# Kernel tuning notes

Hardware: AMD Instinct MI355X
Metric: run time of the kernel (lower is better)

The kernel has to match this reference:

```python
import jax, jax.numpy as jnp
import numpy as np

N_NODES = 100000
N_EDGES = 1600000
N_REL = 4
DIM = 64
N_LAYERS = 3
EPS = 1e-10


def setup_inputs() -> dict:
    key = jax.random.key(0)
    ks = jax.random.split(key, 12)
    node_feat = jax.random.normal(ks[0], (N_NODES, DIM), dtype=jnp.float32)
    edge_weight = jnp.ones((N_EDGES,), dtype=jnp.float32)
    edge_src = jax.random.randint(ks[1], (N_EDGES,), 0, N_NODES, dtype=jnp.int32)
    edge_dst = jax.random.randint(ks[2], (N_EDGES,), 0, N_NODES, dtype=jnp.int32)
    edge_rel = jax.random.randint(ks[3], (N_EDGES,), 0, N_REL, dtype=jnp.int32)
    s = 0.1
    # stacked per-layer parameters (all layers are DIM -> DIM)
    conv_lin_w = jax.random.normal(ks[4], (N_LAYERS, N_REL * DIM, DIM), dtype=jnp.float32) * s
    conv_lin_b = jnp.zeros((N_LAYERS, DIM), dtype=jnp.float32)
    conv_self_w = jax.random.normal(ks[5], (N_LAYERS, DIM, DIM), dtype=jnp.float32) * s
    conv_self_b = jnp.zeros((N_LAYERS, DIM), dtype=jnp.float32)
    hw_proj_w = jax.random.normal(ks[6], (N_LAYERS, 2 * DIM, DIM), dtype=jnp.float32) * s
    hw_proj_b = jnp.zeros((N_LAYERS, DIM), dtype=jnp.float32)
    hw_trans_w = jax.random.normal(ks[7], (N_LAYERS, 2 * DIM, DIM), dtype=jnp.float32) * s
    hw_trans_b = jnp.full((N_LAYERS, DIM), -2.0, dtype=jnp.float32)  # bias.fill_(-2.0)
    return dict(node_feat=node_feat, edge_weight=edge_weight,
                conv_lin_w=conv_lin_w, conv_lin_b=conv_lin_b,
                conv_self_w=conv_self_w, conv_self_b=conv_self_b,
                hw_proj_w=hw_proj_w, hw_proj_b=hw_proj_b,
                hw_trans_w=hw_trans_w, hw_trans_b=hw_trans_b,
                edge_src=edge_src, edge_dst=edge_dst, edge_rel=edge_rel)


def _rgcn(x, ew, src, dst, rel, lin_w, lin_b, self_w, self_b):
    # message: gather source features, weight by edge weight
    msg = x[src] * ew[:, None]                     # [E, D]
    seg = dst * N_REL + rel                        # [E] -> (node, relation) bucket
    num_seg = N_NODES * N_REL
    agg = jax.ops.segment_sum(msg, seg, num_segments=num_seg)        # [N*R, D]
    deg = jax.ops.segment_sum(ew, seg, num_segments=num_seg)         # [N*R]
    upd = (agg / (deg[:, None] + EPS)).reshape(N_NODES, N_REL * DIM)  # [N, R*D]
    out = upd @ lin_w + lin_b + x @ self_w + self_b
    return jax.nn.sigmoid(out)


def _highway(cur, prev, pw, pb, tw, tb):
    cat = jnp.concatenate([cur, prev], axis=1)     # [N, 2D]
    proj = jax.nn.relu(cat @ pw + pb)
    gate = jax.nn.sigmoid(cat @ tw + tb)
    return gate * proj + (1.0 - gate) * cur


def reference(node_feat, edge_weight, conv_lin_w, conv_lin_b, conv_self_w, conv_self_b,
              hw_proj_w, hw_proj_b, hw_trans_w, hw_trans_b, edge_src, edge_dst, edge_rel):
    layer_input = node_feat
    prev_gcn = node_feat
    for i in range(N_LAYERS):
        hidden = _rgcn(layer_input, edge_weight, edge_src, edge_dst, edge_rel,
                       conv_lin_w[i], conv_lin_b[i], conv_self_w[i], conv_self_b[i])
        gated = _highway(hidden, prev_gcn, hw_proj_w[i], hw_proj_b[i],
                         hw_trans_w[i], hw_trans_b[i])
        layer_input = gated
        prev_gcn = hidden
    return layer_input  # node_feature
```

## Files before the change

kernel.cpp:

```cpp
#include <hip/hip_runtime.h>

#define NN   100000
#define NE   1600000
#define NB   400000
#define EPS  1e-10f

#define NPB   32
#define NCHK  256
#define EPC   6250
#define NBUCK 391
#define NHBC  (NBUCK * NCHK)
#define NSCAN (NB + NHBC)
#define NBLK_FUSED 489
#define KB_CAP 4608

typedef __attribute__((ext_vector_type(8))) short bfrag8;
typedef __attribute__((ext_vector_type(4))) float f4acc;

__device__ __forceinline__ unsigned short f2bf(float f) {
    union { float f; unsigned u; } v; v.f = f;
    unsigned r = v.u + 0x7FFF + ((v.u >> 16) & 1);
    return (unsigned short)(r >> 16);
}
__device__ __forceinline__ float bf2f(unsigned short b) {
    union { unsigned u; float f; } v; v.u = ((unsigned)b) << 16;
    return v.f;
}

__global__ __launch_bounds__(256) void kA1(
    const int* __restrict__ dst, const int* __restrict__ rel,
    int* __restrict__ cnt_seg, int* __restrict__ histBC,
    const float* __restrict__ xf, unsigned short* __restrict__ xb)
{
    __shared__ int s_h[NBUCK];
    for (int i = threadIdx.x; i < NBUCK; i += 256) s_h[i] = 0;
    __syncthreads();
    int e0 = blockIdx.x * EPC;
    for (int e = e0 + threadIdx.x; e < e0 + EPC; e += 256) {
        int d = dst[e];
        atomicAdd(&s_h[d >> 8], 1);
        atomicAdd(&cnt_seg[d * 4 + rel[e]], 1);
    }
    __syncthreads();
    for (int i = threadIdx.x; i < NBUCK; i += 256)
        histBC[i * NCHK + blockIdx.x] = s_h[i];

    for (int c = blockIdx.x * 256 + threadIdx.x; c < NN * 8; c += NCHK * 256) {
        const float4* s4 = (const float4*)xf + (size_t)c * 2;
        float4 a = s4[0], b = s4[1];
        unsigned short r[8] = { f2bf(a.x), f2bf(a.y), f2bf(a.z), f2bf(a.w),
                                f2bf(b.x), f2bf(b.y), f2bf(b.z), f2bf(b.w) };
        *(uint4*)(xb + (size_t)c * 8) = *(const uint4*)r;
    }
}

__global__ __launch_bounds__(1024) void k_scan_local_g(
    const int* __restrict__ in, int* __restrict__ out,
    int* __restrict__ blksum, int n)
{
    __shared__ int s[1024];
    int t = threadIdx.x;
    int i = blockIdx.x * 1024 + t;
    int v = (i < n) ? in[i] : 0;
    s[t] = v;
    __syncthreads();
    #pragma unroll
    for (int off = 1; off < 1024; off <<= 1) {
        int u = (t >= off) ? s[t - off] : 0;
        __syncthreads();
        s[t] += u;
        __syncthreads();
    }
    if (i < n) out[i] = s[t] - v;
    if (t == 1023) blksum[blockIdx.x] = s[t];
}

__global__ __launch_bounds__(512) void k_scan_blk_g(
    int* __restrict__ blksum, int* __restrict__ blkoff, int nblk)
{
    __shared__ int s[512];
    int t = threadIdx.x;
    int v = (t < nblk) ? blksum[t] : 0;
    s[t] = v;
    __syncthreads();
    #pragma unroll
    for (int off = 1; off < 512; off <<= 1) {
        int u = (t >= off) ? s[t - off] : 0;
        __syncthreads();
        s[t] += u;
        __syncthreads();
    }
    if (t < nblk) blkoff[t] = s[t] - v;
}

__global__ __launch_bounds__(1024) void k_scan_add_g(
    int* __restrict__ out, const int* __restrict__ blkoff, int n)
{
    int i = blockIdx.x * 1024 + threadIdx.x;
    if (i < n) out[i] += blkoff[blockIdx.x];
}

__global__ __launch_bounds__(256) void kA3(
    const int* __restrict__ src, const int* __restrict__ dst,
    const int* __restrict__ rel, const float* __restrict__ ew,
    const int* __restrict__ chunkOff, int2* __restrict__ pA)
{
    __shared__ int s_c[NBUCK];
    for (int i = threadIdx.x; i < NBUCK; i += 256)
        s_c[i] = chunkOff[i * NCHK + blockIdx.x] - NE;
    __syncthreads();
    int e0 = blockIdx.x * EPC;
    for (int e = e0 + threadIdx.x; e < e0 + EPC; e += 256) {
        int d = dst[e], r = rel[e];
        int pos = atomicAdd(&s_c[d >> 8], 1);
        int2 v;
        v.x = src[e] | (((d & 255) * 4 + r) << 20);
        v.y = __float_as_int(ew[e]);
        pA[pos] = v;
    }
}

__global__ __launch_bounds__(256) void kB(
    const int* __restrict__ row_ptr, const int2* __restrict__ pA,
    int2* __restrict__ edat)
{
    __shared__ int2 s_e[KB_CAP];
    __shared__ int s_c[1024];
    __shared__ int s_p[256];
    const int b    = blockIdx.x;
    const int t    = threadIdx.x;
    const int seg0 = b * 1024;
    const int segN = min(1024, NB - seg0);
    const int pbeg = row_ptr[seg0];
    const int pend = row_ptr[seg0 + segN];

    for (int i = t; i < 1024; i += 256) s_c[i] = 0;
    __syncthreads();
    for (int p = pbeg + t; p < pend; p += 256) {
        int2 v = pA[p];
        int idx = p - pbeg;
        if (idx < KB_CAP) s_e[idx] = v;
        atomicAdd(&s_c[((unsigned)v.x) >> 20], 1);
    }
    __syncthreads();

    int c0 = s_c[t * 4], c1 = s_c[t * 4 + 1], c2 = s_c[t * 4 + 2], c3 = s_c[t * 4 + 3];
    int tsum = c0 + c1 + c2 + c3;
    s_p[t] = tsum;
    __syncthreads();
    #pragma unroll
    for (int off = 1; off < 256; off <<= 1) {
        int u = (t >= off) ? s_p[t - off] : 0;
        __syncthreads();
        s_p[t] += u;
        __syncthreads();
    }
    int base = s_p[t] - tsum;
    s_c[t * 4]     = base;
    s_c[t * 4 + 1] = base + c0;
    s_c[t * 4 + 2] = base + c0 + c1;
    s_c[t * 4 + 3] = base + c0 + c1 + c2;
    __syncthreads();

    for (int p = pbeg + t; p < pend; p += 256) {
        int idx = p - pbeg;
        int2 v = (idx < KB_CAP) ? s_e[idx] : pA[p];
        int sl = ((unsigned)v.x) >> 20;
        int pos = atomicAdd(&s_c[sl], 1);
        int2 o; o.x = v.x & 0xFFFFF; o.y = v.y;
        edat[pbeg + pos] = o;
    }
    if (b == 0 && t < 192) { int2 z; z.x = 0; z.y = 0; edat[NE + t] = z; }
}

__global__ __launch_bounds__(256) void k_cvt_w(
    const float* __restrict__ lin_w, const float* __restrict__ self_w,
    const float* __restrict__ pw, const float* __restrict__ tw,
    unsigned short* __restrict__ WL, unsigned short* __restrict__ WP,
    unsigned short* __restrict__ WT2)
{
    int id = blockIdx.x * 256 + threadIdx.x;
    if (id >= 3 * 64 * 576) return;
    int i = id / (64 * 576);
    int r = id % (64 * 576);
    int j = r / 576;
    int k = r % 576;
    if (k < 320) {
        float v = (k < 256) ? lin_w[((size_t)i * 256 + k) * 64 + j]
                            : self_w[((size_t)i * 64 + (k - 256)) * 64 + j];
        WL[((size_t)i * 64 + j) * 320 + k] = f2bf(v);
    } else if (k < 448) {
        int kk = k - 320;
        WP[((size_t)i * 64 + j) * 128 + kk] = f2bf(pw[((size_t)i * 128 + kk) * 64 + j]);
    } else {
        int kk = k - 448;
        WT2[((size_t)i * 64 + j) * 128 + kk] = f2bf(tw[((size_t)i * 128 + kk) * 64 + j]);
    }
}

template<int LBASE>
__device__ __forceinline__ void gather16(
    unsigned short (&g)[16], int2 mb,
    const unsigned short* __restrict__ xb, int lane)
{
    #pragma unroll
    for (int j = 0; j < 16; ++j) {
        unsigned sm = (unsigned)__builtin_amdgcn_readlane(mb.x, LBASE + j);
        g[j] = xb[((size_t)sm << 6) + lane];
    }
}

template<int LBASE, bool CHECK>
__device__ __forceinline__ void consume16(
    const unsigned short (&g)[16], int2 mb, int ebase,
    int E1, int& seg, int& segEnd,
    float& acc, float& dsum,
    const int* sRP, int sbase, int wid, int lane, char* sAp)
{
    #pragma unroll
    for (int j = 0; j < 16; ++j) {
        int eidx = ebase + j;
        if (!CHECK || eidx < E1) {
            while (eidx >= segEnd) {
                float u = acc * __builtin_amdgcn_rcpf(dsum + EPS);
                int ln = wid * 8 + (seg >> 2);
                int cb = ((seg & 3) * 64 + lane) * 2;
                *(unsigned short*)(sAp + ln * 640 + (cb ^ ((ln & 7) << 4))) = f2bf(u);
                acc = 0.f; dsum = 0.f;
                ++seg;
                segEnd = __builtin_amdgcn_readfirstlane(sRP[sbase + seg + 1]);
            }
            float w = __int_as_float(__builtin_amdgcn_readlane(mb.y, LBASE + j));
            acc = fmaf(bf2f(g[j]), w, acc);
            dsum += w;
        }
    }
}

template<bool CHECK>
__device__ __forceinline__ void agg_iter64(
    unsigned short (&ga)[16], unsigned short (&gb)[16],
    int2& mb, int e, int E1, int& seg, int& segEnd,
    float& acc, float& dsum, const int* sRP, int sbase,
    int wid, int lane, char* sAp,
    const unsigned short* __restrict__ xb, const int2* __restrict__ edat)
{
    int2 mbn = edat[e + 64 + lane];
    gather16<16>(gb, mb, xb, lane);
    consume16<0, CHECK>(ga, mb, e, E1, seg, segEnd, acc, dsum, sRP, sbase, wid, lane, sAp);
    gather16<32>(ga, mb, xb, lane);
    consume16<16, CHECK>(gb, mb, e + 16, E1, seg, segEnd, acc, dsum, sRP, sbase, wid, lane, sAp);
    gather16<48>(gb, mb, xb, lane);
    consume16<32, CHECK>(ga, mb, e + 32, E1, seg, segEnd, acc, dsum, sRP, sbase, wid, lane, sAp);
    gather16<0>(ga, mbn, xb, lane);
    consume16<48, CHECK>(gb, mb, e + 48, E1, seg, segEnd, acc, dsum, sRP, sbase, wid, lane, sAp);
    mb = mbn;
}

__global__ __launch_bounds__(256, 5) void k_layer(
    const unsigned short* __restrict__ xb,
    const unsigned short* __restrict__ prevb,
    const int* __restrict__ row_ptr,
    const int2* __restrict__ edat,
    const unsigned short* __restrict__ WL,
    const unsigned short* __restrict__ WP,
    const unsigned short* __restrict__ WT2,
    const float* __restrict__ lin_b, const float* __restrict__ self_b,
    const float* __restrict__ pb, const float* __restrict__ tb,
    unsigned short* __restrict__ hidb,
    unsigned short* __restrict__ gatedb,
    float* __restrict__ outf,
    int last)
{
    __shared__ __align__(16) unsigned short sA[NPB * 320];
    __shared__ __align__(16) unsigned short sH[NPB * 128];
    __shared__ int sRP[NPB * 4 + 1];

    const int tid  = threadIdx.x;
    const int lane = tid & 63;
    const int wid  = tid >> 6;
    const int n0   = blockIdx.x * NPB;
    const int bcol = wid * 16 + (lane & 15);
    const int koff2 = (lane >> 4) * 16;
    const int arow = lane & 15;
    const int hi   = lane >> 4;

    if (tid < NPB * 4 + 1) sRP[tid] = row_ptr[n0 * 4 + tid];

    {
        int r  = tid >> 3;
        int c0 = (tid & 7) * 8;
        uint4 pv = *(const uint4*)&prevb[(size_t)(n0 + r) * 64 + c0];
        int swz = (r & 7) << 4;
        *(uint4*)((char*)sH + r * 256 + (((64 + c0) * 2) ^ swz)) = pv;
        uint4 xv = *(const uint4*)&xb[(size_t)(n0 + r) * 64 + c0];
        *(uint4*)((char*)sA + r * 640 + (((256 + c0) * 2) ^ swz)) = xv;
    }

    __syncthreads();

    const int sbase = wid * 32;
    int E0 = __builtin_amdgcn_readfirstlane(sRP[sbase]);
    int E1 = __builtin_amdgcn_readfirstlane(sRP[sbase + 32]);
    int seg = 0;
    int segEnd = __builtin_amdgcn_readfirstlane(sRP[sbase + 1]);
    float acc = 0.f, dsum = 0.f;

    int2 mb = edat[E0 + lane];
    unsigned short ga[16], gb[16];
    gather16<0>(ga, mb, xb, lane);

    int e = E0;
    for (; e + 64 <= E1; e += 64)
        agg_iter64<false>(ga, gb, mb, e, E1, seg, segEnd, acc, dsum,
                          sRP, sbase, wid, lane, (char*)sA, xb, edat);
    if (e < E1)
        agg_iter64<true>(ga, gb, mb, e, E1, seg, segEnd, acc, dsum,
                         sRP, sbase, wid, lane, (char*)sA, xb, edat);

    while (seg < 32) {
        float u = acc * __builtin_amdgcn_rcpf(dsum + EPS);
        int ln = wid * 8 + (seg >> 2);
        int cb = ((seg & 3) * 64 + lane) * 2;
        *(unsigned short*)((char*)sA + ln * 640 + (cb ^ ((ln & 7) << 4))) = f2bf(u);
        acc = 0.f; dsum = 0.f;
        ++seg;
    }

    bfrag8 bwL[10];
    #pragma unroll
    for (int ks = 0; ks < 10; ++ks)
        bwL[ks] = *(const bfrag8*)((const char*)WL + bcol * 640 + ks * 64 + koff2);
    float biasC = lin_b[bcol] + self_b[bcol];
    float pbv = pb[bcol], tbv = tb[bcol];

    __syncthreads();

    f4acc accC0 = {0.f, 0.f, 0.f, 0.f};
    f4acc accC1 = {0.f, 0.f, 0.f, 0.f};
    #pragma unroll
    for (int ks = 0; ks < 10; ++ks) {
        int co = ks * 64 + koff2;
        bfrag8 a0 = *(const bfrag8*)((const char*)sA + arow * 640 +
                                     (co ^ ((arow & 7) << 4)));
        bfrag8 a1 = *(const bfrag8*)((const char*)sA + (16 + arow) * 640 +
                                     (co ^ (((16 + arow) & 7) << 4)));
        accC0 = __builtin_amdgcn_mfma_f32_16x16x32_bf16(a0, bwL[ks], accC0, 0, 0, 0);
        accC1 = __builtin_amdgcn_mfma_f32_16x16x32_bf16(a1, bwL[ks], accC1, 0, 0, 0);
    }

    bfrag8 bwP[4], bwT[4];
    #pragma unroll
    for (int ks = 0; ks < 4; ++ks) {
        bwP[ks] = *(const bfrag8*)((const char*)WP  + bcol * 256 + ks * 64 + koff2);
        bwT[ks] = *(const bfrag8*)((const char*)WT2 + bcol * 256 + ks * 64 + koff2);
    }

    float hid[8];
    #pragma unroll
    for (int rt = 0; rt < 2; ++rt) {
        #pragma unroll
        for (int q = 0; q < 4; ++q) {
            float o = (rt == 0 ? accC0[q] : accC1[q]) + biasC;
            float h = 1.f / (1.f + __expf(-o));
            hid[rt * 4 + q] = h;
            int row = rt * 16 + hi * 4 + q;
            unsigned short hb = f2bf(h);
            *(unsigned short*)((char*)sH + row * 256 +
                               ((bcol * 2) ^ ((row & 7) << 4))) = hb;
            hidb[(size_t)(n0 + row) * 64 + bcol] = hb;
        }
    }

    __syncthreads();

    f4acc accP0 = {0.f, 0.f, 0.f, 0.f};
    f4acc accP1 = {0.f, 0.f, 0.f, 0.f};
    f4acc accT0 = {0.f, 0.f, 0.f, 0.f};
    f4acc accT1 = {0.f, 0.f, 0.f, 0.f};
    #pragma unroll
    for (int ks = 0; ks < 4; ++ks) {
        int co = ks * 64 + koff2;
        bfrag8 a0 = *(const bfrag8*)((const char*)sH + arow * 256 +
                                     (co ^ ((arow & 7) << 4)));
        bfrag8 a1 = *(const bfrag8*)((const char*)sH + (16 + arow) * 256 +
                                     (co ^ (((16 + arow) & 7) << 4)));
        accP0 = __builtin_amdgcn_mfma_f32_16x16x32_bf16(a0, bwP[ks], accP0, 0, 0, 0);
        accP1 = __builtin_amdgcn_mfma_f32_16x16x32_bf16(a1, bwP[ks], accP1, 0, 0, 0);
        accT0 = __builtin_amdgcn_mfma_f32_16x16x32_bf16(a0, bwT[ks], accT0, 0, 0, 0);
        accT1 = __builtin_amdgcn_mfma_f32_16x16x32_bf16(a1, bwT[ks], accT1, 0, 0, 0);
    }

    #pragma unroll
    for (int rt = 0; rt < 2; ++rt) {
        #pragma unroll
        for (int q = 0; q < 4; ++q) {
            float ap = (rt == 0 ? accP0[q] : accP1[q]);
            float at = (rt == 0 ? accT0[q] : accT1[q]);
            float proj = fmaxf(ap + pbv, 0.f);
            float gate = 1.f / (1.f + __expf(-(at + tbv)));
            float o = gate * proj + (1.f - gate) * hid[rt * 4 + q];
            int row = rt * 16 + hi * 4 + q;
            if (last) outf[(size_t)(n0 + row) * 64 + bcol] = o;
            else      gatedb[(size_t)(n0 + row) * 64 + bcol] = f2bf(o);
        }
    }
}

extern "C" void kernel_launch(void* const* d_in, const int* in_sizes, int n_in,
                              void* d_out, int out_size, void* d_ws, size_t ws_size,
                              hipStream_t stream)
{
    const float* node_feat = (const float*)d_in[0];
    const float* ew        = (const float*)d_in[1];
    const float* lin_w     = (const float*)d_in[2];
    const float* lin_b     = (const float*)d_in[3];
    const float* self_w    = (const float*)d_in[4];
    const float* self_b    = (const float*)d_in[5];
    const float* pw        = (const float*)d_in[6];
    const float* pb        = (const float*)d_in[7];
    const float* tw        = (const float*)d_in[8];
    const float* tb        = (const float*)d_in[9];
    const int*   src       = (const int*)d_in[10];
    const int*   dst       = (const int*)d_in[11];
    const int*   rel       = (const int*)d_in[12];
    float* outf = (float*)d_out;

    char* ws = (char*)d_ws;
    int*            scanout  = (int*)(ws + 0);
    int*            cnt_cat  = (int*)(ws + 2000640);
    int*            blksum   = (int*)(ws + 4001280);
    int*            blkoff   = (int*)(ws + 4003328);
    int2*           pA       = (int2*)(ws + 4005888);
    int2*           edat     = (int2*)(ws + 16805888);
    unsigned short* nfb      = (unsigned short*)(ws + 29607424);
    unsigned short* hbfA     = (unsigned short*)(ws + 42407424);
    unsigned short* hbfB     = (unsigned short*)(ws + 55207424);
    unsigned short* gbfA     = (unsigned short*)(ws + 68007424);
    unsigned short* gbfB     = (unsigned short*)(ws + 80807424);
    unsigned short* WL       = (unsigned short*)(ws + 93607424);
    unsigned short* WP       = (unsigned short*)(ws + 93607424 + 122880);
    unsigned short* WT2      = (unsigned short*)(ws + 93607424 + 122880 + 49152);

    int* row_ptr  = scanout;
    int* chunkOff = scanout + NB;
    int* cnt_seg  = cnt_cat;
    int* histBC   = cnt_cat + NB;

    hipMemsetAsync(cnt_cat, 0, NSCAN * sizeof(int), stream);
    kA1<<<NCHK, 256, 0, stream>>>(dst, rel, cnt_seg, histBC, node_feat, nfb);
    k_scan_local_g<<<NBLK_FUSED, 1024, 0, stream>>>(cnt_cat, scanout, blksum, NSCAN);
    k_scan_blk_g<<<1, 512, 0, stream>>>(blksum, blkoff, NBLK_FUSED);
    k_scan_add_g<<<NBLK_FUSED, 1024, 0, stream>>>(scanout, blkoff, NSCAN);
    kA3<<<NCHK, 256, 0, stream>>>(src, dst, rel, ew, chunkOff, pA);
    kB<<<NBUCK, 256, 0, stream>>>(row_ptr, pA, edat);

    k_cvt_w<<<432, 256, 0, stream>>>(lin_w, self_w, pw, tw, WL, WP, WT2);

    const unsigned short* cur  = nfb;
    const unsigned short* prev = nfb;
    unsigned short* hbuf[3] = { hbfA, hbfB, hbfA };
    unsigned short* gbuf[3] = { gbfA, gbfB, gbfA };

    for (int i = 0; i < 3; ++i) {
        int lastL = (i == 2);
        k_layer<<<NN / NPB, 256, 0, stream>>>(
            cur, prev, row_ptr, edat,
            WL  + (size_t)i * 64 * 320,
            WP  + (size_t)i * 64 * 128,
            WT2 + (size_t)i * 64 * 128,
            lin_b + (size_t)i * 64, self_b + (size_t)i * 64,
            pb + (size_t)i * 64, tb + (size_t)i * 64,
            hbuf[i], gbuf[i], outf, lastL);
        cur  = gbuf[i];
        prev = hbuf[i];
    }
}
```

Baseline: 325.4 us.

## Derive row pointers in bucket sort instead of global per-segment count scan

Drops the global atomic per-(node,relation) segment counting and the large scan over 400k segment counts. Only the bucket/chunk histogram is scanned, and each bucket-sort block writes row_ptr from its local prefix sums. The 1.6M global atomics, the memset and most of the scan traffic go away. kB gains an extra pass that writes row pointers.

```diff
diff --git a/kernel.cpp b/kernel.cpp
--- a/kernel.cpp
+++ b/kernel.cpp
@@ -10,8 +10,7 @@
 #define EPC   6250
 #define NBUCK 391
 #define NHBC  (NBUCK * NCHK)
-#define NSCAN (NB + NHBC)
-#define NBLK_FUSED 489
+#define NBLK_H 98
 #define KB_CAP 4608
 
 typedef __attribute__((ext_vector_type(8))) short bfrag8;
@@ -28,19 +27,16 @@
 }
 
 __global__ __launch_bounds__(256) void kA1(
-    const int* __restrict__ dst, const int* __restrict__ rel,
-    int* __restrict__ cnt_seg, int* __restrict__ histBC,
+    const int* __restrict__ dst,
+    int* __restrict__ histBC,
     const float* __restrict__ xf, unsigned short* __restrict__ xb)
 {
     __shared__ int s_h[NBUCK];
     for (int i = threadIdx.x; i < NBUCK; i += 256) s_h[i] = 0;
     __syncthreads();
     int e0 = blockIdx.x * EPC;
-    for (int e = e0 + threadIdx.x; e < e0 + EPC; e += 256) {
-        int d = dst[e];
-        atomicAdd(&s_h[d >> 8], 1);
-        atomicAdd(&cnt_seg[d * 4 + rel[e]], 1);
-    }
+    for (int e = e0 + threadIdx.x; e < e0 + EPC; e += 256)
+        atomicAdd(&s_h[dst[e] >> 8], 1);
     __syncthreads();
     for (int i = threadIdx.x; i < NBUCK; i += 256)
         histBC[i * NCHK + blockIdx.x] = s_h[i];
@@ -107,7 +103,7 @@
 {
     __shared__ int s_c[NBUCK];
     for (int i = threadIdx.x; i < NBUCK; i += 256)
-        s_c[i] = chunkOff[i * NCHK + blockIdx.x] - NE;
+        s_c[i] = chunkOff[i * NCHK + blockIdx.x];
     __syncthreads();
     int e0 = blockIdx.x * EPC;
     for (int e = e0 + threadIdx.x; e < e0 + EPC; e += 256) {
@@ -121,8 +117,8 @@
 }
 
 __global__ __launch_bounds__(256) void kB(
-    const int* __restrict__ row_ptr, const int2* __restrict__ pA,
-    int2* __restrict__ edat)
+    const int* __restrict__ chunkOff, const int2* __restrict__ pA,
+    int2* __restrict__ edat, int* __restrict__ row_ptr)
 {
     __shared__ int2 s_e[KB_CAP];
     __shared__ int s_c[1024];
@@ -131,8 +127,8 @@
     const int t    = threadIdx.x;
     const int seg0 = b * 1024;
     const int segN = min(1024, NB - seg0);
-    const int pbeg = row_ptr[seg0];
-    const int pend = row_ptr[seg0 + segN];
+    const int pbeg = chunkOff[b * NCHK];
+    const int pend = (b + 1 < NBUCK) ? chunkOff[(b + 1) * NCHK] : NE;
 
     for (int i = t; i < 1024; i += 256) s_c[i] = 0;
     __syncthreads();
@@ -160,6 +156,11 @@
     s_c[t * 4 + 1] = base + c0;
     s_c[t * 4 + 2] = base + c0 + c1;
     s_c[t * 4 + 3] = base + c0 + c1 + c2;
+    __syncthreads();
+
+    for (int i = t; i < segN; i += 256)
+        row_ptr[seg0 + i] = pbeg + s_c[i];
+    if (b == NBUCK - 1 && t == 0) row_ptr[NB] = NE;
     __syncthreads();
 
     for (int p = pbeg + t; p < pend; p += 256) {
@@ -427,33 +428,28 @@
     float* outf = (float*)d_out;
 
     char* ws = (char*)d_ws;
-    int*            scanout  = (int*)(ws + 0);
-    int*            cnt_cat  = (int*)(ws + 2000640);
-    int*            blksum   = (int*)(ws + 4001280);
-    int*            blkoff   = (int*)(ws + 4003328);
-    int2*           pA       = (int2*)(ws + 4005888);
-    int2*           edat     = (int2*)(ws + 16805888);
-    unsigned short* nfb      = (unsigned short*)(ws + 29607424);
-    unsigned short* hbfA     = (unsigned short*)(ws + 42407424);
-    unsigned short* hbfB     = (unsigned short*)(ws + 55207424);
-    unsigned short* gbfA     = (unsigned short*)(ws + 68007424);
-    unsigned short* gbfB     = (unsigned short*)(ws + 80807424);
-    unsigned short* WL       = (unsigned short*)(ws + 93607424);
-    unsigned short* WP       = (unsigned short*)(ws + 93607424 + 122880);
-    unsigned short* WT2      = (unsigned short*)(ws + 93607424 + 122880 + 49152);
-
-    int* row_ptr  = scanout;
-    int* chunkOff = scanout + NB;
-    int* cnt_seg  = cnt_cat;
-    int* histBC   = cnt_cat + NB;
-
-    hipMemsetAsync(cnt_cat, 0, NSCAN * sizeof(int), stream);
-    kA1<<<NCHK, 256, 0, stream>>>(dst, rel, cnt_seg, histBC, node_feat, nfb);
-    k_scan_local_g<<<NBLK_FUSED, 1024, 0, stream>>>(cnt_cat, scanout, blksum, NSCAN);
-    k_scan_blk_g<<<1, 512, 0, stream>>>(blksum, blkoff, NBLK_FUSED);
-    k_scan_add_g<<<NBLK_FUSED, 1024, 0, stream>>>(scanout, blkoff, NSCAN);
+    int*            row_ptr  = (int*)(ws + 0);
+    int*            chunkOff = (int*)(ws + 1600256);
+    int*            histBC   = (int*)(ws + 2000640);
+    int*            blksum   = (int*)(ws + 2401024);
+    int*            blkoff   = (int*)(ws + 2403072);
+    int2*           pA       = (int2*)(ws + 2405376);
+    int2*           edat     = (int2*)(ws + 15205376);
+    unsigned short* nfb      = (unsigned short*)(ws + 28007424);
+    unsigned short* hbfA     = (unsigned short*)(ws + 40807424);
+    unsigned short* hbfB     = (unsigned short*)(ws + 53607424);
+    unsigned short* gbfA     = (unsigned short*)(ws + 66407424);
+    unsigned short* gbfB     = (unsigned short*)(ws + 79207424);
+    unsigned short* WL       = (unsigned short*)(ws + 92007424);
+    unsigned short* WP       = (unsigned short*)(ws + 92007424 + 122880);
+    unsigned short* WT2      = (unsigned short*)(ws + 92007424 + 122880 + 49152);
+
+    kA1<<<NCHK, 256, 0, stream>>>(dst, histBC, node_feat, nfb);
+    k_scan_local_g<<<NBLK_H, 1024, 0, stream>>>(histBC, chunkOff, blksum, NHBC);
+    k_scan_blk_g<<<1, 512, 0, stream>>>(blksum, blkoff, NBLK_H);
+    k_scan_add_g<<<NBLK_H, 1024, 0, stream>>>(chunkOff, blkoff, NHBC);
     kA3<<<NCHK, 256, 0, stream>>>(src, dst, rel, ew, chunkOff, pA);
-    kB<<<NBUCK, 256, 0, stream>>>(row_ptr, pA, edat);
+    kB<<<NBUCK, 256, 0, stream>>>(chunkOff, pA, edat, row_ptr);
 
     k_cvt_w<<<432, 256, 0, stream>>>(lin_w, self_w, pw, tw, WL, WP, WT2);
 
```

Result: faster. 264.4 us (-18.8%).
